# Kernel tuning notes

Measured on AMD Instinct MI355X. Metric: run time of the kernel, lower is better.

## Reference

```python
import jax, jax.numpy as jnp
import numpy as np

B = 1024
INPUT_DIM = 768
NUM_CLASSES = 5
NUM_PRIMARY_CAPS = 32
PRIMARY_CAP_DIM = 8
ROUTING_CAP_DIM = 16
NUM_ITER = 3
PROJ_DIM = 256 * 6 * 6  # 9216
NUM_IN_CAPS = NUM_PRIMARY_CAPS * 16  # conv output is 4x4 spatial -> 512


def squash(t, axis=-1):
    sq = jnp.sum(t * t, axis=axis, keepdims=True)
    scale = sq / (1.0 + sq)
    return scale * t / jnp.sqrt(sq + 1e-8)


def setup_inputs() -> dict:
    key = jax.random.key(0)
    k = jax.random.split(key, 6)
    x = jax.random.normal(k[0], (B, INPUT_DIM), dtype=jnp.float32)
    W1 = jax.random.normal(k[1], (INPUT_DIM, PROJ_DIM), dtype=jnp.float32) * 0.02
    b1 = jnp.zeros((PROJ_DIM,), dtype=jnp.float32)
    convW = jax.random.normal(k[2], (NUM_PRIMARY_CAPS * PRIMARY_CAP_DIM, 256, 3, 3), dtype=jnp.float32) * 0.02  # OIHW
    convB = jnp.zeros((NUM_PRIMARY_CAPS * PRIMARY_CAP_DIM,), dtype=jnp.float32)
    # matches torch.randn init in RoutingCapsules: [num_in, num_out, out_dim, in_dim]
    Wr = jax.random.normal(k[3], (NUM_IN_CAPS, NUM_CLASSES, ROUTING_CAP_DIM, PRIMARY_CAP_DIM), dtype=jnp.float32)
    return {"x": x, "W1": W1, "b1": b1, "convW": convW, "convB": convB, "Wr": Wr}


def reference(x, W1, b1, convW, convB, Wr):
    # feature projection (dropout is identity in eval)
    h = jax.nn.relu(x @ W1 + b1)
    h = h.reshape(-1, 256, 6, 6)
    # primary capsules conv: k=3, s=1, pad=0 -> [B, 256, 4, 4]
    out = jax.lax.conv_general_dilated(h, convW, window_strides=(1, 1), padding='VALID',
                                       dimension_numbers=('NCHW', 'OIHW', 'NCHW'))
    out = out + convB[None, :, None, None]
    bsz = out.shape[0]
    out = out.reshape(bsz, NUM_PRIMARY_CAPS, PRIMARY_CAP_DIM, -1)      # [B,32,8,16]
    out = jnp.transpose(out, (0, 1, 3, 2)).reshape(bsz, -1, PRIMARY_CAP_DIM)  # [B,512,8]
    u = squash(out, axis=-1)
    # prediction vectors u_hat: [B, in_caps, out_caps, out_dim]
    u_hat = jnp.einsum('nodi,bni->bnod', Wr, u)
    # dynamic routing
    b_logits = jnp.zeros((bsz, NUM_IN_CAPS, NUM_CLASSES, 1), dtype=u_hat.dtype)
    v = None
    for it in range(NUM_ITER):
        c = jax.nn.softmax(b_logits, axis=2)
        s = jnp.sum(c * u_hat, axis=1)  # [B, out_caps, out_dim]
        v = squash(s, axis=-1)
        if it < NUM_ITER - 1:
            agreement = jnp.sum(u_hat * v[:, None], axis=-1, keepdims=True)
            b_logits = b_logits + agreement
    class_probs = jnp.sqrt(jnp.sum(v * v, axis=-1))
    return (class_probs, v)
```

## Files before the change

kernel.cpp:

```cpp
#include <hip/hip_runtime.h>
#include <hip/hip_fp16.h>

#define BSZ   1024
#define INDIM 768
#define PROJ  9216
#define NCAP  512
#define NCLS  5
#define K2    2304

typedef __bf16    bf16x8 __attribute__((ext_vector_type(8)));
typedef _Float16  f16x8  __attribute__((ext_vector_type(8)));
typedef float     f32x4  __attribute__((ext_vector_type(4)));
typedef _Float16  h2     __attribute__((ext_vector_type(2)));

static __device__ __forceinline__ unsigned short f2bf(float f) {
  unsigned int x = __float_as_uint(f);
  return (unsigned short)((x + 0x7fffu + ((x >> 16) & 1u)) >> 16);
}
static __device__ __forceinline__ float bf2f(unsigned int u) {
  return __uint_as_float(u << 16);
}

#if defined(__has_builtin)
#if __has_builtin(__builtin_amdgcn_fdot2)
#define HAVE_FDOT2 1
#endif
#endif
static __device__ __forceinline__ float fdot2(h2 a, h2 b, float c) {
#ifdef HAVE_FDOT2
  return __builtin_amdgcn_fdot2(a, b, c, false);
#else
  return c + (float)a[0] * (float)b[0] + (float)a[1] * (float)b[1];
#endif
}
static __device__ __forceinline__ h2 u2h2(unsigned int u) {
  return __builtin_bit_cast(h2, u);
}

static __device__ __forceinline__ void gload16(const void* g, void* l) {
  auto gp = reinterpret_cast<const unsigned int __attribute__((address_space(1)))*>(
      (unsigned long long)g);
  auto lp = reinterpret_cast<unsigned int __attribute__((address_space(3)))*>(
      (unsigned long long)l);
  __builtin_amdgcn_global_load_lds(gp, lp, 16, 0, 0);
}

template <int RELU, int OBF16>
__global__ __launch_bounds__(256) void mfma_gemm(
    const unsigned short* __restrict__ A,
    const unsigned short* __restrict__ Bt,
    const float* __restrict__ bias,
    void* __restrict__ Cout,
    int M, int N, int K) {
  __shared__ __align__(16) unsigned short smem[16384];
  const int t    = threadIdx.x;
  const int bn   = blockIdx.x * 128;
  const int bm   = blockIdx.y * 128;
  const int lane = t & 63;
  const int wid  = t >> 6;
  const int wm   = (wid >> 1) * 64;
  const int wn   = (wid & 1) * 64;
  const int l15  = lane & 15;
  const int kb   = lane >> 4;

  const int r0 = t >> 2,         kc = t & 3;
  const int r1 = (t + 256) >> 2;
  const int gk0 = ((kc ^ (r0 & 3)) << 3);
  const int gk1 = ((kc ^ (r1 & 3)) << 3);

  const unsigned short* Ar0 = A  + (size_t)(bm + r0) * K + gk0;
  const unsigned short* Ar1 = A  + (size_t)(bm + r1) * K + gk1;
  const unsigned short* Br0 = Bt + (size_t)(bn + r0) * K + gk0;
  const unsigned short* Br1 = Bt + (size_t)(bn + r1) * K + gk1;

  int aoff[4], boff[4];
#pragma unroll
  for (int i = 0; i < 4; ++i) {
    const int ra = wm + i * 16 + l15;
    aoff[i] = ra * 32 + ((kb ^ (ra & 3)) << 3);
    const int rb = wn + i * 16 + l15;
    boff[i] = 4096 + rb * 32 + ((kb ^ (rb & 3)) << 3);
  }

  f32x4 acc[4][4];
#pragma unroll
  for (int i = 0; i < 4; ++i)
#pragma unroll
    for (int j = 0; j < 4; ++j)
#pragma unroll
      for (int q = 0; q < 4; ++q) acc[i][j][q] = 0.f;

  const int nk = K >> 5;
  gload16(Ar0, &smem[t * 8]);
  gload16(Ar1, &smem[(t + 256) * 8]);
  gload16(Br0, &smem[4096 + t * 8]);
  gload16(Br1, &smem[4096 + (t + 256) * 8]);
  __syncthreads();

  int buf = 0;
  for (int ks = 0; ks < nk; ++ks) {
    if (ks + 1 < nk) {
      const int k = (ks + 1) << 5;
      const int o = (buf ^ 1) * 8192;
      gload16(Ar0 + k, &smem[o + t * 8]);
      gload16(Ar1 + k, &smem[o + (t + 256) * 8]);
      gload16(Br0 + k, &smem[o + 4096 + t * 8]);
      gload16(Br1 + k, &smem[o + 4096 + (t + 256) * 8]);
    }
    const unsigned short* base = &smem[buf * 8192];
    bf16x8 af[4], bfr[4];
#pragma unroll
    for (int i = 0; i < 4; ++i) {
      af[i]  = *(const bf16x8*)(base + aoff[i]);
      bfr[i] = *(const bf16x8*)(base + boff[i]);
    }
#pragma unroll
    for (int i = 0; i < 4; ++i)
#pragma unroll
      for (int j = 0; j < 4; ++j)
        acc[i][j] = __builtin_amdgcn_mfma_f32_16x16x32_bf16(af[i], bfr[j], acc[i][j], 0, 0, 0);
    __syncthreads();
    buf ^= 1;
  }

#pragma unroll
  for (int j = 0; j < 4; ++j) {
    const int col = bn + wn + j * 16 + l15;
    const float bv = bias[col];
#pragma unroll
    for (int i = 0; i < 4; ++i) {
#pragma unroll
      for (int q = 0; q < 4; ++q) {
        const int row = bm + wm + i * 16 + kb * 4 + q;
        float v = acc[i][j][q] + bv;
        if (RELU) v = fmaxf(v, 0.f);
        if (OBF16) ((unsigned short*)Cout)[(size_t)row * N + col] = f2bf(v);
        else       ((float*)Cout)[(size_t)row * N + col] = v;
      }
    }
  }
}

__global__ __launch_bounds__(256) void conv_gemm(
    const unsigned short* __restrict__ ht,
    const unsigned short* __restrict__ Wt2,
    const float* __restrict__ convB,
    float* __restrict__ cv) {
  __shared__ __align__(16) unsigned short smem[12288];
  const int t    = threadIdx.x;
  const int bn   = blockIdx.x * 128;
  const int bm   = blockIdx.y * 64;
  const int lane = t & 63, wid = t >> 6;
  const int l15  = lane & 15, kb = lane >> 4;

  const int ar  = t >> 2, asg = t & 3;
  const int ab  = (bm + ar) >> 4, ap = (bm + ar) & 15;
  const int spb = (ap >> 2) * 6 + (ap & 3);
  const unsigned short* abase =
      ht + (size_t)ab * PROJ + spb * 256 + ((asg ^ (ar & 3)) << 3);

  const int br0 = t >> 2, br1 = (t + 256) >> 2, bsg = t & 3;
  const unsigned short* bb0 = Wt2 + (size_t)(bn + br0) * K2 + ((bsg ^ (br0 & 3)) << 3);
  const unsigned short* bb1 = Wt2 + (size_t)(bn + br1) * K2 + ((bsg ^ (br1 & 3)) << 3);

  int aoff[4], boff[2];
#pragma unroll
  for (int i = 0; i < 4; ++i) {
    const int ra = i * 16 + l15;
    aoff[i] = ra * 32 + ((kb ^ (ra & 3)) << 3);
  }
#pragma unroll
  for (int j = 0; j < 2; ++j) {
    const int rb = wid * 32 + j * 16 + l15;
    boff[j] = 2048 + rb * 32 + ((kb ^ (rb & 3)) << 3);
  }

  f32x4 acc[4][2];
#pragma unroll
  for (int i = 0; i < 4; ++i)
#pragma unroll
    for (int j = 0; j < 2; ++j)
#pragma unroll
      for (int q = 0; q < 4; ++q) acc[i][j][q] = 0.f;

  auto stage = [&](int ks, int buf) {
    const int tap = ks >> 3;
    const int dsp = tap + 3 * (tap / 3);
    const int ic0 = (ks & 7) << 5;
    unsigned short* sb = &smem[buf * 6144];
    gload16(abase + dsp * 256 + ic0, sb + t * 8);
    gload16(bb0 + ks * 32, sb + 2048 + t * 8);
    gload16(bb1 + ks * 32, sb + 2048 + (t + 256) * 8);
  };

  stage(0, 0);
  __syncthreads();

  int buf = 0;
  for (int ks = 0; ks < 72; ++ks) {
    if (ks + 1 < 72) stage(ks + 1, buf ^ 1);
    const unsigned short* base = &smem[buf * 6144];
    bf16x8 af[4], bfr[2];
#pragma unroll
    for (int i = 0; i < 4; ++i) af[i] = *(const bf16x8*)(base + aoff[i]);
#pragma unroll
    for (int j = 0; j < 2; ++j) bfr[j] = *(const bf16x8*)(base + boff[j]);
#pragma unroll
    for (int i = 0; i < 4; ++i)
#pragma unroll
      for (int j = 0; j < 2; ++j)
        acc[i][j] = __builtin_amdgcn_mfma_f32_16x16x32_bf16(af[i], bfr[j], acc[i][j], 0, 0, 0);
    __syncthreads();
    buf ^= 1;
  }

#pragma unroll
  for (int j = 0; j < 2; ++j) {
    const int col = bn + wid * 32 + j * 16 + l15;
    const float bv = convB[col];
#pragma unroll
    for (int i = 0; i < 4; ++i)
#pragma unroll
      for (int q = 0; q < 4; ++q) {
        const int row = bm + i * 16 + kb * 4 + q;
        cv[(size_t)row * 256 + col] = acc[i][j][q] + bv;
      }
  }
}

__global__ __launch_bounds__(256) void convert_bf16(const float* __restrict__ in,
                                                    unsigned short* __restrict__ out,
                                                    int n4) {
  const int i = blockIdx.x * 256 + threadIdx.x;
  if (i >= n4) return;
  float4 v = ((const float4*)in)[i];
  ushort4 o;
  o.x = f2bf(v.x); o.y = f2bf(v.y); o.z = f2bf(v.z); o.w = f2bf(v.w);
  ((ushort4*)out)[i] = o;
}

__global__ __launch_bounds__(256) void convert_f16(const float* __restrict__ in,
                                                   __half2* __restrict__ out, int n4) {
  const int i = blockIdx.x * 256 + threadIdx.x;
  if (i >= n4) return;
  float4 v = ((const float4*)in)[i];
  out[i * 2]     = __floats2half2_rn(v.x, v.y);
  out[i * 2 + 1] = __floats2half2_rn(v.z, v.w);
}

__global__ __launch_bounds__(256) void transpose_w1_perm(const float* __restrict__ W,
                                                         unsigned short* __restrict__ Wt) {
  __shared__ float tile[32][33];
  const int n0 = blockIdx.x * 32, k0 = blockIdx.y * 32;
  const int r = threadIdx.x >> 3, c = (threadIdx.x & 7) * 4;
  float4 v = *(const float4*)(W + (size_t)(k0 + r) * PROJ + n0 + c);
  tile[r][c] = v.x; tile[r][c + 1] = v.y; tile[r][c + 2] = v.z; tile[r][c + 3] = v.w;
  __syncthreads();
  ushort4 o;
  o.x = f2bf(tile[c + 0][r]); o.y = f2bf(tile[c + 1][r]);
  o.z = f2bf(tile[c + 2][r]); o.w = f2bf(tile[c + 3][r]);
  const int nn = n0 + r;
  const int prow = (nn % 36) * 256 + nn / 36;
  *(ushort4*)(Wt + (size_t)prow * INDIM + k0 + c) = o;
}

__global__ __launch_bounds__(256) void perm_bias(const float* __restrict__ b1,
                                                 float* __restrict__ pb1) {
  const int n = blockIdx.x * 256 + threadIdx.x;
  if (n >= PROJ) return;
  pb1[(n % 36) * 256 + n / 36] = b1[n];
}

__global__ __launch_bounds__(256) void convw_prep2(const float* __restrict__ W,
                                                   unsigned short* __restrict__ Wt2) {
  const int id = blockIdx.x * 256 + threadIdx.x;
  const int oc = id >> 8, ic = id & 255;
  const float* s = W + (size_t)id * 9;
#pragma unroll
  for (int tap = 0; tap < 9; ++tap)
    Wt2[(size_t)oc * K2 + tap * 256 + ic] = f2bf(s[tap]);
}

__global__ __launch_bounds__(256) void squash_u(const float* __restrict__ cv,
                                                __half2* __restrict__ U) {
  const int b = blockIdx.x;
  const int t = threadIdx.x;
#pragma unroll
  for (int h = 0; h < 2; ++h) {
    const int id = t + h * 256;
    const int cap = id & 31, p = id >> 5;
    const float* s = cv + ((size_t)b * 16 + p) * 256 + cap * 8;
    float4 a = *(const float4*)s;
    float4 c = *(const float4*)(s + 4);
    float sq = a.x * a.x + a.y * a.y + a.z * a.z + a.w * a.w +
               c.x * c.x + c.y * c.y + c.z * c.z + c.w * c.w;
    const float scale = sq / (1.f + sq) / sqrtf(sq + 1e-8f);
    __half2* d = U + ((size_t)b * 4096 + cap * 128 + p * 8) / 2;
    d[0] = __floats2half2_rn(a.x * scale, a.y * scale);
    d[1] = __floats2half2_rn(a.z * scale, a.w * scale);
    d[2] = __floats2half2_rn(c.x * scale, c.y * scale);
    d[3] = __floats2half2_rn(c.z * scale, c.w * scale);
  }
}

__global__ __launch_bounds__(256) void uhat_gemm(
    const unsigned short* __restrict__ U,
    const unsigned short* __restrict__ Wrh,
    unsigned short* __restrict__ uhat,
    float* __restrict__ s0q,
    int b0, int CB) {
  __shared__ float sred[4][16][80];
  const int mt = blockIdx.x, q = blockIdx.y;
  const int t = threadIdx.x, wid = t >> 6, lane = t & 63;
  const int l15 = lane & 15, kb = lane >> 4;
  const int bm = mt * 16;
  const int gb = b0 + bm;

  f32x4 sacc[5];
#pragma unroll
  for (int j = 0; j < 5; ++j)
#pragma unroll
    for (int r = 0; r < 4; ++r) sacc[j][r] = 0.f;

  const uint4 zz = make_uint4(0, 0, 0, 0);
  for (int i = 0; i < 32; ++i) {
    const int n = q * 128 + wid * 32 + i;
    uint4 av = zz;
    if (kb == 0) av = *(const uint4*)(U + (size_t)(gb + l15) * 4096 + n * 8);
    const f16x8 af = __builtin_bit_cast(f16x8, av);
    f32x4 cfr[5];
#pragma unroll
    for (int jn = 0; jn < 5; ++jn) {
      uint4 bv = zz;
      if (kb == 0) bv = *(const uint4*)(Wrh + (size_t)n * 640 + (jn * 16 + l15) * 8);
      f32x4 z;
      z[0] = 0.f; z[1] = 0.f; z[2] = 0.f; z[3] = 0.f;
      cfr[jn] = __builtin_amdgcn_mfma_f32_16x16x32_f16(af, __builtin_bit_cast(f16x8, bv), z, 0, 0, 0);
    }
#pragma unroll
    for (int jn = 0; jn < 5; ++jn) {
#pragma unroll
      for (int qq = 0; qq < 4; ++qq) {
        const int row = kb * 4 + qq;
        uhat[(size_t)(bm + row) * 40960 + n * 80 + jn * 16 + l15] =
            __builtin_bit_cast(unsigned short, (_Float16)cfr[jn][qq]);
        sacc[jn][qq] += cfr[jn][qq];
      }
    }
  }
#pragma unroll
  for (int jn = 0; jn < 5; ++jn)
#pragma unroll
    for (int qq = 0; qq < 4; ++qq)
      sred[wid][kb * 4 + qq][jn * 16 + l15] = sacc[jn][qq];
  __syncthreads();
#pragma unroll
  for (int k = 0; k < 5; ++k) {
    const int id = t + k * 256;
    const int r = id / 80, col = id % 80;
    const float val = sred[0][r][col] + sred[1][r][col] + sred[2][r][col] + sred[3][r][col];
    s0q[((size_t)q * CB + bm + r) * 80 + col] = val;
  }
}

template <int MODE>
__global__ __launch_bounds__(256) void route_pass(
    const unsigned short* __restrict__ uhat,
    const float* __restrict__ s0q,
    const float* __restrict__ vsum_in,
    float* __restrict__ vsum_out,
    float* __restrict__ out,
    int b0, int CB) {
  __shared__ unsigned int vph2[40];
  __shared__ float red[4][2][40];
  const int bl = blockIdx.x;
  const int b  = b0 + bl;
  const int t  = threadIdx.x;

  float v0r = 0.f;
  if (t < 80) {
    if (MODE == 1) {
      float s = 0.2f * (s0q[(size_t)bl * 80 + t] +
                        s0q[((size_t)CB + bl) * 80 + t] +
                        s0q[((size_t)2 * CB + bl) * 80 + t] +
                        s0q[((size_t)3 * CB + bl) * 80 + t]);
      float sq = s * s;
      sq += __shfl_xor(sq, 1);
      sq += __shfl_xor(sq, 2);
      sq += __shfl_xor(sq, 4);
      sq += __shfl_xor(sq, 8);
      const float scale = sq / (1.f + sq) / sqrtf(sq + 1e-8f);
      v0r = s * scale;
    } else {
      v0r = vsum_in[(size_t)bl * 80 + t];
    }
    const float vnext = __shfl_down(v0r, 1);
    if ((t & 1) == 0)
      vph2[t >> 1] = __builtin_bit_cast(unsigned int, __floats2half2_rn(v0r, vnext));
  }
  __syncthreads();

  const int p = t >> 1, h = t & 1;
  float acc[5][8];
#pragma unroll
  for (int o = 0; o < 5; ++o)
#pragma unroll
    for (int j = 0; j < 8; ++j) acc[o][j] = 0.f;

  const unsigned short* ub = uhat + (size_t)bl * 40960;
  for (int c4 = 0; c4 < 4; ++c4) {
    const int n = c4 * 128 + p;
    const unsigned short* row = ub + n * 80 + h * 8;
    uint4 uv[5];
#pragma unroll
    for (int o = 0; o < 5; ++o) uv[o] = *(const uint4*)(row + o * 16);
    float ap[5];
#pragma unroll
    for (int o = 0; o < 5; ++o) {
      const int vb = o * 8 + h * 4;
      float a = fdot2(u2h2(uv[o].x), u2h2(vph2[vb]), 0.f);
      a = fdot2(u2h2(uv[o].y), u2h2(vph2[vb + 1]), a);
      a = fdot2(u2h2(uv[o].z), u2h2(vph2[vb + 2]), a);
      a = fdot2(u2h2(uv[o].w), u2h2(vph2[vb + 3]), a);
      ap[o] = a + __shfl_xor(a, 1);
    }
    float m = ap[0];
#pragma unroll
    for (int o = 1; o < 5; ++o) m = fmaxf(m, ap[o]);
    float es = 0.f, e[5];
#pragma unroll
    for (int o = 0; o < 5; ++o) { e[o] = __expf(ap[o] - m); es += e[o]; }
    const float inv = 1.f / es;
#pragma unroll
    for (int o = 0; o < 5; ++o) {
      const float cc = e[o] * inv;
      h2 hx = u2h2(uv[o].x), hy = u2h2(uv[o].y), hz = u2h2(uv[o].z), hw = u2h2(uv[o].w);
      acc[o][0] += cc * (float)hx[0]; acc[o][1] += cc * (float)hx[1];
      acc[o][2] += cc * (float)hy[0]; acc[o][3] += cc * (float)hy[1];
      acc[o][4] += cc * (float)hz[0]; acc[o][5] += cc * (float)hz[1];
      acc[o][6] += cc * (float)hw[0]; acc[o][7] += cc * (float)hw[1];
    }
  }

#pragma unroll
  for (int off = 2; off <= 32; off <<= 1)
#pragma unroll
    for (int o = 0; o < 5; ++o)
#pragma unroll
      for (int j = 0; j < 8; ++j) acc[o][j] += __shfl_xor(acc[o][j], off);
  const int wid = t >> 6, lane = t & 63;
  if (lane < 2) {
#pragma unroll
    for (int o = 0; o < 5; ++o)
#pragma unroll
      for (int j = 0; j < 8; ++j) red[wid][lane][o * 8 + j] = acc[o][j];
  }
  __syncthreads();

  if (t < 80) {
    const int o = t >> 4, d = t & 15, hh = d >> 3, dl = d & 7;
    const int c = o * 8 + dl;
    float s = red[0][hh][c] + red[1][hh][c] + red[2][hh][c] + red[3][hh][c];
    float sq = s * s;
    sq += __shfl_xor(sq, 1);
    sq += __shfl_xor(sq, 2);
    sq += __shfl_xor(sq, 4);
    sq += __shfl_xor(sq, 8);
    const float scale = sq / (1.f + sq) / sqrtf(sq + 1e-8f);
    const float vn = s * scale;
    if (MODE == 1) {
      vsum_out[(size_t)bl * 80 + t] = v0r + vn;
    } else {
      out[5 * BSZ + (size_t)b * 80 + t] = vn;
      float vv = vn * vn;
      vv += __shfl_xor(vv, 1);
      vv += __shfl_xor(vv, 2);
      vv += __shfl_xor(vv, 4);
      vv += __shfl_xor(vv, 8);
      if ((t & 15) == 0) out[(size_t)b * 5 + o] = sqrtf(vv);
    }
  }
}

extern "C" void kernel_launch(void* const* d_in, const int* in_sizes, int n_in,
                              void* d_out, int out_size, void* d_ws, size_t ws_size,
                              hipStream_t stream) {
  const float* x     = (const float*)d_in[0];
  const float* W1    = (const float*)d_in[1];
  const float* b1    = (const float*)d_in[2];
  const float* convW = (const float*)d_in[3];
  const float* convB = (const float*)d_in[4];
  const float* Wr    = (const float*)d_in[5];
  float* out = (float*)d_out;

  char* base = (char*)d_ws;
  size_t off = 0;
  auto alloc = [&](size_t bytes) { size_t o = off; off = (off + bytes + 255) & ~(size_t)255; return o; };
  const size_t o_wrh  = alloc((size_t)NCAP * 640 * 2);
  const size_t o_u    = alloc((size_t)BSZ * 4096 * 2);
  const size_t o_s0q  = alloc((size_t)4 * BSZ * 80 * 4);
  const size_t o_vsum = alloc((size_t)BSZ * 80 * 4);
  const size_t o_pool = off;
  size_t poff = o_pool;
  auto palloc = [&](size_t bytes) { size_t o = poff; poff = (poff + bytes + 255) & ~(size_t)255; return o; };
  const size_t o_ht  = palloc((size_t)BSZ * PROJ * 2);
  const size_t o_w1t = palloc((size_t)PROJ * INDIM * 2);
  const size_t o_xb  = palloc((size_t)BSZ * INDIM * 2);
  const size_t o_wt2 = palloc((size_t)256 * K2 * 2);
  const size_t o_pb1 = palloc((size_t)PROJ * 4);
  const size_t o_cv  = palloc((size_t)BSZ * 16 * 256 * 4);

  unsigned short* ht   = (unsigned short*)(base + o_ht);
  unsigned short* w1t  = (unsigned short*)(base + o_w1t);
  unsigned short* xb   = (unsigned short*)(base + o_xb);
  unsigned short* wt2  = (unsigned short*)(base + o_wt2);
  float*          pb1  = (float*)(base + o_pb1);
  unsigned short* wrh  = (unsigned short*)(base + o_wrh);
  float*          cv   = (float*)(base + o_cv);
  __half2*        u    = (__half2*)(base + o_u);
  float*          s0q  = (float*)(base + o_s0q);
  float*          vsum = (float*)(base + o_vsum);
  unsigned short* uhat = (unsigned short*)(base + o_pool);

  convert_bf16<<<(BSZ * INDIM / 4 + 255) / 256, 256, 0, stream>>>(x, xb, BSZ * INDIM / 4);
  transpose_w1_perm<<<dim3(PROJ / 32, INDIM / 32), 256, 0, stream>>>(W1, w1t);
  perm_bias<<<PROJ / 256, 256, 0, stream>>>(b1, pb1);
  convw_prep2<<<256, 256, 0, stream>>>(convW, wt2);
  convert_f16<<<(NCAP * 640 / 4 + 255) / 256, 256, 0, stream>>>(Wr, (__half2*)wrh, NCAP * 640 / 4);

  mfma_gemm<1, 1><<<dim3(PROJ / 128, BSZ / 128), 256, 0, stream>>>(
      xb, w1t, pb1, (void*)ht, BSZ, PROJ, INDIM);

  conv_gemm<<<dim3(2, 256), 256, 0, stream>>>(ht, wt2, convB, cv);

  squash_u<<<BSZ, 256, 0, stream>>>(cv, u);

  const size_t pool_sz = ws_size > o_pool ? ws_size - o_pool : 0;
  int CB = 1024;
  while (CB > 16 && (size_t)CB * 512 * 80 * 2 > pool_sz) CB >>= 1;
  for (int b0 = 0; b0 < BSZ; b0 += CB) {
    uhat_gemm<<<dim3(CB / 16, 4), 256, 0, stream>>>(
        (const unsigned short*)u, wrh, uhat, s0q, b0, CB);
    route_pass<1><<<CB, 256, 0, stream>>>(uhat, s0q, nullptr, vsum, out, b0, CB);
    route_pass<2><<<CB, 256, 0, stream>>>(uhat, nullptr, vsum, nullptr, out, b0, CB);
  }
}
```

Measured before the change: 181.7 us.

## Store conv output as fp16 and restructure uhat GEMM for vectorized stores

The conv GEMM now writes its output in fp16 instead of fp32, halving the traffic into squash_u. The uhat GEMM swaps the MFMA operands so each lane holds four consecutive output dims, and writes them as one 8-byte ushort4 store instead of scattered 2-byte stores. It also runs 512 threads per block over an 8-way capsule split with an unrolled 8-step inner loop, and the partial sums in s0q grow from 4 to 8 slices. Costs are an fp16 rounding of the conv output before squash and more partial-sum reads in route_pass.

```diff
diff --git a/kernel.cpp b/kernel.cpp
--- a/kernel.cpp
+++ b/kernel.cpp
@@ -35,6 +35,9 @@
 }
 static __device__ __forceinline__ h2 u2h2(unsigned int u) {
   return __builtin_bit_cast(h2, u);
+}
+static __device__ __forceinline__ unsigned short f2h(float f) {
+  return __builtin_bit_cast(unsigned short, (_Float16)f);
 }
 
 static __device__ __forceinline__ void gload16(const void* g, void* l) {
@@ -145,7 +148,7 @@
     const unsigned short* __restrict__ ht,
     const unsigned short* __restrict__ Wt2,
     const float* __restrict__ convB,
-    float* __restrict__ cv) {
+    unsigned short* __restrict__ cv) {
   __shared__ __align__(16) unsigned short smem[12288];
   const int t    = threadIdx.x;
   const int bn   = blockIdx.x * 128;
@@ -223,7 +226,7 @@
 #pragma unroll
       for (int q = 0; q < 4; ++q) {
         const int row = bm + i * 16 + kb * 4 + q;
-        cv[(size_t)row * 256 + col] = acc[i][j][q] + bv;
+        cv[(size_t)row * 256 + col] = f2h(acc[i][j][q] + bv);
       }
   }
 }
@@ -281,7 +284,7 @@
     Wt2[(size_t)oc * K2 + tap * 256 + ic] = f2bf(s[tap]);
 }
 
-__global__ __launch_bounds__(256) void squash_u(const float* __restrict__ cv,
+__global__ __launch_bounds__(256) void squash_u(const unsigned short* __restrict__ cv,
                                                 __half2* __restrict__ U) {
   const int b = blockIdx.x;
   const int t = threadIdx.x;
@@ -289,27 +292,29 @@
   for (int h = 0; h < 2; ++h) {
     const int id = t + h * 256;
     const int cap = id & 31, p = id >> 5;
-    const float* s = cv + ((size_t)b * 16 + p) * 256 + cap * 8;
-    float4 a = *(const float4*)s;
-    float4 c = *(const float4*)(s + 4);
-    float sq = a.x * a.x + a.y * a.y + a.z * a.z + a.w * a.w +
-               c.x * c.x + c.y * c.y + c.z * c.z + c.w * c.w;
+    const unsigned short* s = cv + ((size_t)b * 16 + p) * 256 + cap * 8;
+    uint4 qv = *(const uint4*)s;
+    h2 a0 = u2h2(qv.x), a1 = u2h2(qv.y), a2 = u2h2(qv.z), a3 = u2h2(qv.w);
+    float f0 = a0[0], f1 = a0[1], f2 = a1[0], f3 = a1[1];
+    float f4 = a2[0], f5 = a2[1], f6 = a3[0], f7 = a3[1];
+    float sq = f0 * f0 + f1 * f1 + f2 * f2 + f3 * f3 +
+               f4 * f4 + f5 * f5 + f6 * f6 + f7 * f7;
     const float scale = sq / (1.f + sq) / sqrtf(sq + 1e-8f);
     __half2* d = U + ((size_t)b * 4096 + cap * 128 + p * 8) / 2;
-    d[0] = __floats2half2_rn(a.x * scale, a.y * scale);
-    d[1] = __floats2half2_rn(a.z * scale, a.w * scale);
-    d[2] = __floats2half2_rn(c.x * scale, c.y * scale);
-    d[3] = __floats2half2_rn(c.z * scale, c.w * scale);
-  }
-}
-
-__global__ __launch_bounds__(256) void uhat_gemm(
+    d[0] = __floats2half2_rn(f0 * scale, f1 * scale);
+    d[1] = __floats2half2_rn(f2 * scale, f3 * scale);
+    d[2] = __floats2half2_rn(f4 * scale, f5 * scale);
+    d[3] = __floats2half2_rn(f6 * scale, f7 * scale);
+  }
+}
+
+__global__ __launch_bounds__(512) void uhat_gemm(
     const unsigned short* __restrict__ U,
     const unsigned short* __restrict__ Wrh,
     unsigned short* __restrict__ uhat,
     float* __restrict__ s0q,
     int b0, int CB) {
-  __shared__ float sred[4][16][80];
+  __shared__ float sred[8][16][80];
   const int mt = blockIdx.x, q = blockIdx.y;
   const int t = threadIdx.x, wid = t >> 6, lane = t & 63;
   const int l15 = lane & 15, kb = lane >> 4;
@@ -323,43 +328,44 @@
     for (int r = 0; r < 4; ++r) sacc[j][r] = 0.f;
 
   const uint4 zz = make_uint4(0, 0, 0, 0);
-  for (int i = 0; i < 32; ++i) {
-    const int n = q * 128 + wid * 32 + i;
+#pragma unroll
+  for (int i = 0; i < 8; ++i) {
+    const int n = q * 64 + wid * 8 + i;
     uint4 av = zz;
     if (kb == 0) av = *(const uint4*)(U + (size_t)(gb + l15) * 4096 + n * 8);
-    const f16x8 af = __builtin_bit_cast(f16x8, av);
-    f32x4 cfr[5];
+    const f16x8 uf = __builtin_bit_cast(f16x8, av);
 #pragma unroll
     for (int jn = 0; jn < 5; ++jn) {
-      uint4 bv = zz;
-      if (kb == 0) bv = *(const uint4*)(Wrh + (size_t)n * 640 + (jn * 16 + l15) * 8);
+      uint4 wv = zz;
+      if (kb == 0) wv = *(const uint4*)(Wrh + (size_t)n * 640 + (jn * 16 + l15) * 8);
       f32x4 z;
       z[0] = 0.f; z[1] = 0.f; z[2] = 0.f; z[3] = 0.f;
-      cfr[jn] = __builtin_amdgcn_mfma_f32_16x16x32_f16(af, __builtin_bit_cast(f16x8, bv), z, 0, 0, 0);
-    }
-#pragma unroll
-    for (int jn = 0; jn < 5; ++jn) {
-#pragma unroll
-      for (int qq = 0; qq < 4; ++qq) {
-        const int row = kb * 4 + qq;
-        uhat[(size_t)(bm + row) * 40960 + n * 80 + jn * 16 + l15] =
-            __builtin_bit_cast(unsigned short, (_Float16)cfr[jn][qq]);
-        sacc[jn][qq] += cfr[jn][qq];
-      }
-    }
-  }
+      f32x4 c = __builtin_amdgcn_mfma_f32_16x16x32_f16(
+          __builtin_bit_cast(f16x8, wv), uf, z, 0, 0, 0);
+      ushort4 st;
+      st.x = f2h(c[0]); st.y = f2h(c[1]); st.z = f2h(c[2]); st.w = f2h(c[3]);
+      *(ushort4*)(uhat + ((size_t)(bm + l15) * 512 + n) * 80 + jn * 16 + kb * 4) = st;
+#pragma unroll
+      for (int qq = 0; qq < 4; ++qq) sacc[jn][qq] += c[qq];
+    }
+  }
+
 #pragma unroll
   for (int jn = 0; jn < 5; ++jn)
 #pragma unroll
     for (int qq = 0; qq < 4; ++qq)
-      sred[wid][kb * 4 + qq][jn * 16 + l15] = sacc[jn][qq];
+      sred[wid][l15][jn * 16 + kb * 4 + qq] = sacc[jn][qq];
   __syncthreads();
 #pragma unroll
-  for (int k = 0; k < 5; ++k) {
-    const int id = t + k * 256;
-    const int r = id / 80, col = id % 80;
-    const float val = sred[0][r][col] + sred[1][r][col] + sred[2][r][col] + sred[3][r][col];
-    s0q[((size_t)q * CB + bm + r) * 80 + col] = val;
+  for (int k = 0; k < 3; ++k) {
+    const int id = t + k * 512;
+    if (id < 1280) {
+      const int bb = id / 80, od = id % 80;
+      float val = 0.f;
+#pragma unroll
+      for (int w = 0; w < 8; ++w) val += sred[w][bb][od];
+      s0q[((size_t)q * CB + bm + bb) * 80 + od] = val;
+    }
   }
 }
 
@@ -380,10 +386,10 @@
   float v0r = 0.f;
   if (t < 80) {
     if (MODE == 1) {
-      float s = 0.2f * (s0q[(size_t)bl * 80 + t] +
-                        s0q[((size_t)CB + bl) * 80 + t] +
-                        s0q[((size_t)2 * CB + bl) * 80 + t] +
-                        s0q[((size_t)3 * CB + bl) * 80 + t]);
+      float s = 0.f;
+#pragma unroll
+      for (int g = 0; g < 8; ++g) s += s0q[((size_t)g * CB + bl) * 80 + t];
+      s *= 0.2f;
       float sq = s * s;
       sq += __shfl_xor(sq, 1);
       sq += __shfl_xor(sq, 2);
@@ -498,7 +504,7 @@
   auto alloc = [&](size_t bytes) { size_t o = off; off = (off + bytes + 255) & ~(size_t)255; return o; };
   const size_t o_wrh  = alloc((size_t)NCAP * 640 * 2);
   const size_t o_u    = alloc((size_t)BSZ * 4096 * 2);
-  const size_t o_s0q  = alloc((size_t)4 * BSZ * 80 * 4);
+  const size_t o_s0q  = alloc((size_t)8 * BSZ * 80 * 4);
   const size_t o_vsum = alloc((size_t)BSZ * 80 * 4);
   const size_t o_pool = off;
   size_t poff = o_pool;
@@ -508,7 +514,7 @@
   const size_t o_xb  = palloc((size_t)BSZ * INDIM * 2);
   const size_t o_wt2 = palloc((size_t)256 * K2 * 2);
   const size_t o_pb1 = palloc((size_t)PROJ * 4);
-  const size_t o_cv  = palloc((size_t)BSZ * 16 * 256 * 4);
+  const size_t o_cv  = palloc((size_t)BSZ * 16 * 256 * 2);
 
   unsigned short* ht   = (unsigned short*)(base + o_ht);
   unsigned short* w1t  = (unsigned short*)(base + o_w1t);
@@ -516,7 +522,7 @@
   unsigned short* wt2  = (unsigned short*)(base + o_wt2);
   float*          pb1  = (float*)(base + o_pb1);
   unsigned short* wrh  = (unsigned short*)(base + o_wrh);
-  float*          cv   = (float*)(base + o_cv);
+  unsigned short* cv   = (unsigned short*)(base + o_cv);
   __half2*        u    = (__half2*)(base + o_u);
   float*          s0q  = (float*)(base + o_s0q);
   float*          vsum = (float*)(base + o_vsum);
@@ -539,7 +545,7 @@
   int CB = 1024;
   while (CB > 16 && (size_t)CB * 512 * 80 * 2 > pool_sz) CB >>= 1;
   for (int b0 = 0; b0 < BSZ; b0 += CB) {
-    uhat_gemm<<<dim3(CB / 16, 4), 256, 0, stream>>>(
+    uhat_gemm<<<dim3(CB / 16, 8), 512, 0, stream>>>(
         (const unsigned short*)u, wrh, uhat, s0q, b0, CB);
     route_pass<1><<<CB, 256, 0, stream>>>(uhat, s0q, nullptr, vsum, out, b0, CB);
     route_pass<2><<<CB, 256, 0, stream>>>(uhat, nullptr, vsum, nullptr, out, b0, CB);
```

After: 160.3 us. 1.13x faster.
